# Kernel optimization log

Hardware: AMD Instinct MI355X
Metric: run time of the kernel (lower is better)

Reference implementation:

```python
import jax, jax.numpy as jnp
import numpy as np

N_NODES = 100000
N_EDGES = 3200000
NFEAT = 512
DIMS = [NFEAT, 12, 10, 8, 6, 4, 16]  # layer widths; 16 = nout


def setup_inputs() -> dict:
    key = jax.random.key(0)
    ks = jax.random.split(key, 16)
    inp = {
        "x": jax.random.normal(ks[0], (N_NODES, NFEAT), dtype=jnp.float32),
        "edge_index": jax.random.randint(ks[1], (2, N_EDGES), 0, N_NODES, dtype=jnp.int32),
        "edge_weight": jax.random.uniform(ks[2], (N_EDGES,), dtype=jnp.float32) * (1.0 / 32.0),
    }
    # GCN layer params: support = x @ W; out = adj @ support + b
    for i in range(6):
        fan_in, fan_out = DIMS[i], DIMS[i + 1]
        scale = 1.0 / np.sqrt(fan_in)
        inp[f"W{i+1}"] = jax.random.uniform(ks[3 + 2 * i], (fan_in, fan_out), dtype=jnp.float32, minval=-scale, maxval=scale)
        inp[f"b{i+1}"] = jax.random.uniform(ks[4 + 2 * i], (fan_out,), dtype=jnp.float32, minval=-scale, maxval=scale)
    return inp


def _gcn_layer(h, src, dst, w, W, b):
    # support = h @ W  -> [N, out]; out = A @ support + b via edge scatter-add
    support = h @ W
    msgs = w[:, None] * support[src]            # [E, out]
    agg = jax.ops.segment_sum(msgs, dst, num_segments=N_NODES)
    return agg + b


def reference(x, edge_index, edge_weight, W1, b1, W2, b2, W3, b3, W4, b4, W5, b5, W6, b6):
    src, dst = edge_index[0], edge_index[1]
    # Eval-mode forward: F.dropout(training=False) is identity.
    h = x
    for W, b in ((W1, b1), (W2, b2), (W3, b3), (W4, b4), (W5, b5), (W6, b6)):
        h = _gcn_layer(h, src, dst, edge_weight, W, b)
    return h
```

## Files before the change

### kernel.cpp

```cpp
#include <hip/hip_runtime.h>
#include <hip/hip_fp16.h>

constexpr int NF = 512;
constexpr int SCAN_B = 1024;
constexpr int DPB = 256;
constexpr int CHUNK = 16384;
constexpr int BMAX = 9216;
constexpr float WSCALE = 1048544.0f;
constexpr float WINV = 1.0f / 1048544.0f;

__device__ __forceinline__ float dot16(const float* a, const float* w, float acc) {
#pragma unroll
  for (int j = 0; j < 16; ++j) acc = fmaf(a[j], w[j], acc);
  return acc;
}

template <int COUT>
__global__ __launch_bounds__(256) void gemm_big_count_kernel(
    const float* __restrict__ x, const float* __restrict__ W,
    __half* __restrict__ sup, int n, const int* __restrict__ ei,
    int* __restrict__ cnt, int E, int nbuck, int nch) {
  __shared__ __align__(16) float smem[COUT * NF];
  if ((int)blockIdx.x < nch) {
    int* hist = (int*)smem;
    const int c = blockIdx.x;
    for (int b = threadIdx.x; b < nbuck; b += 256) hist[b] = 0;
    __syncthreads();
    const int base = c * CHUNK;
    for (int i = threadIdx.x; i < CHUNK; i += 256) {
      const int e = base + i;
      if (e < E) atomicAdd(&hist[ei[E + e] >> 8], 1);
    }
    __syncthreads();
    for (int b = threadIdx.x; b < nbuck; b += 256) cnt[b * nch + c] = hist[b];
    return;
  }

  float(*sW)[NF] = (float(*)[NF])smem;
  for (int i = threadIdx.x; i < COUT * NF; i += 256) {
    int c = i / NF, k = i - c * NF;
    sW[c][k] = W[(size_t)k * COUT + c];
  }
  __syncthreads();

  const int v = (blockIdx.x - nch) * 256 + threadIdx.x;
  if (v >= n) return;

  float acc[COUT];
#pragma unroll
  for (int c = 0; c < COUT; ++c) acc[c] = 0.f;

  const float4* xr = (const float4*)(x + (size_t)v * NF);
  float4 cur[4], nxt[4];
#pragma unroll
  for (int j = 0; j < 4; ++j) cur[j] = xr[j];
  for (int kb = 0; kb < NF / 16; ++kb) {
    const int kn = (kb + 1 < NF / 16) ? kb + 1 : kb;
#pragma unroll
    for (int j = 0; j < 4; ++j) nxt[j] = xr[kn * 4 + j];
    const float* af = (const float*)cur;
#pragma unroll
    for (int c = 0; c < COUT; ++c) {
      const float4* wr = (const float4*)(&sW[c][kb * 16]);
      float4 wq[4];
#pragma unroll
      for (int j = 0; j < 4; ++j) wq[j] = wr[j];
      acc[c] = dot16(af, (const float*)wq, acc[c]);
    }
#pragma unroll
    for (int j = 0; j < 4; ++j) cur[j] = nxt[j];
  }

  union { uint4 u; __half2 h[4]; } o1;
  union { uint2 u; __half2 h[2]; } o2;
#pragma unroll
  for (int g = 0; g < 4; ++g) o1.h[g] = __floats2half2_rn(acc[2 * g], acc[2 * g + 1]);
#pragma unroll
  for (int g = 0; g < 2; ++g) o2.h[g] = __floats2half2_rn(acc[8 + 2 * g], acc[9 + 2 * g]);
  __half* o = sup + (size_t)v * 16;
  *(uint4*)o = o1.u;
  *(uint2*)(o + 8) = o2.u;
}


__global__ __launch_bounds__(256) void scan1_kernel(const int* __restrict__ src,
                                                    int* __restrict__ dst,
                                                    int* __restrict__ bsums, int m) {
  __shared__ int s[256];
  const int t = threadIdx.x;
  const int idx = blockIdx.x * SCAN_B + t * 4;
  int4 d = {0, 0, 0, 0};
  if (idx + 3 < m) {
    d = *(const int4*)(src + idx);
  } else {
    if (idx + 0 < m) d.x = src[idx + 0];
    if (idx + 1 < m) d.y = src[idx + 1];
    if (idx + 2 < m) d.z = src[idx + 2];
    if (idx + 3 < m) d.w = src[idx + 3];
  }
  const int sum = d.x + d.y + d.z + d.w;
  s[t] = sum;
  __syncthreads();
  for (int off = 1; off < 256; off <<= 1) {
    int val = (t >= off) ? s[t - off] : 0;
    __syncthreads();
    s[t] += val;
    __syncthreads();
  }
  const int excl = s[t] - sum;
  if (t == 255) bsums[blockIdx.x] = s[255];
  if (idx + 0 < m) dst[idx + 0] = excl;
  if (idx + 1 < m) dst[idx + 1] = excl + d.x;
  if (idx + 2 < m) dst[idx + 2] = excl + d.x + d.y;
  if (idx + 3 < m) dst[idx + 3] = excl + d.x + d.y + d.z;
}

__global__ __launch_bounds__(256) void scan2_kernel(const int* __restrict__ bsums,
                                                    int* __restrict__ bscan, int nb) {
  __shared__ int s[256];
  const int t = threadIdx.x;
  const int v = (t < nb) ? bsums[t] : 0;
  s[t] = v;
  __syncthreads();
  for (int off = 1; off < 256; off <<= 1) {
    int val = (t >= off) ? s[t - off] : 0;
    __syncthreads();
    s[t] += val;
    __syncthreads();
  }
  if (t < nb) bscan[t] = s[t] - v;
}

__global__ __launch_bounds__(256) void scatterC_kernel(
    const int* __restrict__ ei, const float* __restrict__ ew,
    const int* __restrict__ offsp, const int* __restrict__ bscan,
    int2* __restrict__ pairs, int E, int nbuck, int nch) {
  __shared__ int cur[512];
  const int c = blockIdx.x;
  for (int b = threadIdx.x; b < nbuck; b += 256) {
    const int idx = b * nch + c;
    cur[b] = offsp[idx] + bscan[idx >> 10];
  }
  __syncthreads();
  const int base = c * CHUNK;
  for (int i = threadIdx.x; i < CHUNK; i += 256) {
    const int e = base + i;
    if (e >= E) break;
    const int s = ei[e];
    const int d = ei[E + e];
    const float w = ew[e];
    const int pos = atomicAdd(&cur[d >> 8], 1);
    pairs[pos] = make_int2(s | ((d & (DPB - 1)) << 17), __float_as_int(w));
  }
}

__global__ __launch_bounds__(256) void bucketD_kernel(
    const int* __restrict__ offsp, const int* __restrict__ bscan,
    const int2* __restrict__ pairs, unsigned* __restrict__ cpairs,
    int* __restrict__ rowptr, int n, int E, int nbuck, int nch) {
  __shared__ unsigned stage[BMAX];
  __shared__ int h[DPB];
  __shared__ int s[DPB];
  __shared__ int cur[DPB];
  const int b = blockIdx.x;
  const int t = threadIdx.x;
  if (b == 0 && t == 0) rowptr[n] = E;
  const int i0 = b * nch;
  const int base = offsp[i0] + bscan[i0 >> 10];
  int end;
  if (b + 1 < nbuck) {
    const int i1 = (b + 1) * nch;
    end = offsp[i1] + bscan[i1 >> 10];
  } else {
    end = E;
  }
  const int cnt = end - base;

  for (int i = t; i < DPB; i += 256) h[i] = 0;
  __syncthreads();
  for (int i = t; i < cnt; i += 256) {
    const int2 p = pairs[base + i];
    atomicAdd(&h[(p.x >> 17) & (DPB - 1)], 1);
  }
  __syncthreads();
  const int own = h[t];
  s[t] = own;
  __syncthreads();
  for (int off = 1; off < 256; off <<= 1) {
    int val = (t >= off) ? s[t - off] : 0;
    __syncthreads();
    s[t] += val;
    __syncthreads();
  }
  const int excl = s[t] - own;
  cur[t] = excl;
  const int dst = b * DPB + t;
  if (dst < n) rowptr[dst] = base + excl;
  __syncthreads();
  for (int i = t; i < cnt; i += 256) {
    const int2 p = pairs[base + i];
    const int r = atomicAdd(&cur[(p.x >> 17) & (DPB - 1)], 1);
    const float w = __int_as_float(p.y);
    const unsigned wq = (unsigned)__float2int_rn(w * WSCALE);
    if (r < BMAX) stage[r] = (unsigned)(p.x & 0x1FFFF) | (wq << 17);
  }
  __syncthreads();
  const int lim = cnt < BMAX ? cnt : BMAX;
  for (int i = t; i < lim; i += 256) cpairs[base + i] = stage[i];
}


template <int PIN, int CIN>
__device__ __forceinline__ void load_row_h(const __half* __restrict__ sup,
                                           unsigned p, float* hv, float* wout) {
  *wout = (float)(p >> 17) * WINV;
  const __half* hr = sup + (size_t)(p & 0x1FFFF) * PIN;
  __half2 h[6];
  if constexpr (PIN == 16) {
    union { uint4 u; __half2 h[4]; } a;
    union { uint2 u; __half2 h[2]; } b;
    a.u = *(const uint4*)hr;
    b.u = *(const uint2*)(hr + 8);
    h[0] = a.h[0]; h[1] = a.h[1]; h[2] = a.h[2]; h[3] = a.h[3];
    h[4] = b.h[0]; h[5] = b.h[1];
  } else if constexpr (PIN == 8) {
    union { uint4 u; __half2 h[4]; } a;
    a.u = *(const uint4*)hr;
    h[0] = a.h[0]; h[1] = a.h[1]; h[2] = a.h[2]; h[3] = a.h[3];
  } else {
    union { uint2 u; __half2 h[2]; } a;
    a.u = *(const uint2*)hr;
    h[0] = a.h[0]; h[1] = a.h[1];
  }
#pragma unroll
  for (int g = 0; g < CIN / 2; ++g) {
    float2 f = __half22float2(h[g]);
    hv[2 * g] = f.x;
    hv[2 * g + 1] = f.y;
  }
}

template <int PIN, int CIN, int COUT, int POUT, bool AGG_BIAS, bool OUT_BIAS,
          bool IDENT, typename TOUT>
__global__ __launch_bounds__(256) void pull_one_kernel(
    const int* __restrict__ rowptr, const unsigned* __restrict__ cp,
    const __half* __restrict__ sup, const float* __restrict__ bagg,
    const float* __restrict__ W, const float* __restrict__ bout,
    TOUT* __restrict__ outp, int n) {
  __shared__ float sW[IDENT ? 1 : CIN * 16];
  __shared__ float sba[16];
  __shared__ float sbo[16];
  const int tt = threadIdx.x;
  if constexpr (!IDENT) {
    for (int i = tt; i < CIN * 16; i += 256) {
      const int k = i >> 4, j = i & 15;
      sW[i] = (j < COUT) ? W[k * COUT + j] : 0.f;
    }
  }
  if constexpr (AGG_BIAS)
    if (tt < CIN) sba[tt] = bagg[tt];
  if constexpr (OUT_BIAS)
    if (tt < COUT) sbo[tt] = bout[tt];
  __syncthreads();

  const int gt = blockIdx.x * 256 + tt;
  const int v = gt >> 3;
  const int lane = gt & 7;
  if (v >= n) return;
  const int beg = rowptr[v];
  const int end = rowptr[v + 1];

  float acc[CIN];
#pragma unroll
  for (int c = 0; c < CIN; ++c) acc[c] = 0.f;

  for (int base = beg; base < end; base += 32) {
    const int i = base + 4 * lane;
    unsigned pq[4] = {0u, 0u, 0u, 0u};
    if (i < end) __builtin_memcpy(pq, cp + i, 16);
    const unsigned p0 = (i + 0 < end) ? pq[0] : 0u;
    const unsigned p1 = (i + 1 < end) ? pq[1] : 0u;
    const unsigned p2 = (i + 2 < end) ? pq[2] : 0u;
    const unsigned p3 = (i + 3 < end) ? pq[3] : 0u;
    float w0, w1, w2, w3, h0[CIN], h1[CIN], h2[CIN], h3[CIN];
    load_row_h<PIN, CIN>(sup, p0, h0, &w0);
    load_row_h<PIN, CIN>(sup, p1, h1, &w1);
    load_row_h<PIN, CIN>(sup, p2, h2, &w2);
    load_row_h<PIN, CIN>(sup, p3, h3, &w3);
#pragma unroll
    for (int c = 0; c < CIN; ++c) acc[c] = fmaf(w0, h0[c], acc[c]);
#pragma unroll
    for (int c = 0; c < CIN; ++c) acc[c] = fmaf(w1, h1[c], acc[c]);
#pragma unroll
    for (int c = 0; c < CIN; ++c) acc[c] = fmaf(w2, h2[c], acc[c]);
#pragma unroll
    for (int c = 0; c < CIN; ++c) acc[c] = fmaf(w3, h3[c], acc[c]);
  }

#pragma unroll
  for (int c = 0; c < CIN; ++c) {
    acc[c] += __shfl_xor(acc[c], 1);
    acc[c] += __shfl_xor(acc[c], 2);
    acc[c] += __shfl_xor(acc[c], 4);
    if constexpr (AGG_BIAS) acc[c] += sba[c];
  }

  if constexpr (IDENT) {
    if (lane == 0) {
      union { uint2 u; __half2 h[2]; } o;
      o.h[0] = __floats2half2_rn(acc[0], acc[1]);
      o.h[1] = __floats2half2_rn(acc[2], acc[3]);
      *(uint2*)((__half*)outp + (size_t)v * POUT) = o.u;
    }
  } else {
    if (lane * 4 < POUT) {
      const int col = lane * 4;
      float r[4];
#pragma unroll
      for (int j = 0; j < 4; ++j) {
        float a = OUT_BIAS ? sbo[col + j] : 0.f;
#pragma unroll
        for (int k = 0; k < CIN; ++k) a = fmaf(acc[k], sW[k * 16 + col + j], a);
        r[j] = a;
      }
      if constexpr (sizeof(TOUT) == 2) {
        union { uint2 u; __half2 h[2]; } o;
        o.h[0] = __floats2half2_rn(r[0], r[1]);
        o.h[1] = __floats2half2_rn(r[2], r[3]);
        *(uint2*)((__half*)outp + (size_t)v * POUT + col) = o.u;
      } else {
        float4 o;
        o.x = r[0]; o.y = r[1]; o.z = r[2]; o.w = r[3];
        *(float4*)((float*)outp + (size_t)v * POUT + col) = o;
      }
    }
  }
}

extern "C" void kernel_launch(void* const* d_in, const int* in_sizes, int n_in,
                              void* d_out, int out_size, void* d_ws,
                              size_t ws_size, hipStream_t stream) {
  const float* x = (const float*)d_in[0];
  const int* ei = (const int*)d_in[1];
  const float* ew = (const float*)d_in[2];
  const float* W1 = (const float*)d_in[3];
  const float* b1 = (const float*)d_in[4];
  const float* W2 = (const float*)d_in[5];
  const float* b2 = (const float*)d_in[6];
  const float* W3 = (const float*)d_in[7];
  const float* b3 = (const float*)d_in[8];
  const float* W4 = (const float*)d_in[9];
  const float* b4 = (const float*)d_in[10];
  const float* W5 = (const float*)d_in[11];
  const float* b5 = (const float*)d_in[12];
  const float* W6 = (const float*)d_in[13];
  const float* b6 = (const float*)d_in[14];
  float* out = (float*)d_out;

  const int n = in_sizes[0] / NF;
  const int E = in_sizes[2];

  const int nbuck = (n + DPB - 1) / DPB;
  const int nch = (E + CHUNK - 1) / CHUNK;
  const int M = nbuck * nch;
  const int Mpad = (M + 3) & ~3;

  __half* A = (__half*)d_ws;
  __half* B = A + (size_t)n * 16;
  int* cnt = (int*)(B + (size_t)n * 16);
  int* offs = cnt + Mpad;
  int* bsums = offs + Mpad;
  int* bscan = bsums + 256;
  int* rowptr = bscan + 256;
  uintptr_t up = (uintptr_t)(rowptr + n + 1);
  up = (up + 15) & ~(uintptr_t)15;
  unsigned* cpairs = (unsigned*)up;
  int2* pairs = (int2*)(cpairs + E);

  const int gn256 = (n + 255) / 256;
  const int nsb = (M + SCAN_B - 1) / SCAN_B;
  const int gq8 = (n * 8 + 255) / 256;

  gemm_big_count_kernel<12>
      <<<nch + gn256, 256, 0, stream>>>(x, W1, A, n, ei, cnt, E, nbuck, nch);
  scan1_kernel<<<nsb, 256, 0, stream>>>(cnt, offs, bsums, M);
  scan2_kernel<<<1, 256, 0, stream>>>(bsums, bscan, nsb);
  scatterC_kernel<<<nch, 256, 0, stream>>>(ei, ew, offs, bscan, pairs, E, nbuck, nch);
  bucketD_kernel<<<nbuck, 256, 0, stream>>>(offs, bscan, pairs, cpairs, rowptr,
                                            n, E, nbuck, nch);

  pull_one_kernel<16, 12, 10, 16, true, false, false, __half>
      <<<gq8, 256, 0, stream>>>(rowptr, cpairs, A, b1, W2, nullptr, B, n);
  pull_one_kernel<16, 10, 8, 8, true, false, false, __half>
      <<<gq8, 256, 0, stream>>>(rowptr, cpairs, B, b2, W3, nullptr, A, n);
  pull_one_kernel<8, 8, 6, 8, true, false, false, __half>
      <<<gq8, 256, 0, stream>>>(rowptr, cpairs, A, b3, W4, nullptr, B, n);
  pull_one_kernel<8, 6, 4, 4, true, false, false, __half>
      <<<gq8, 256, 0, stream>>>(rowptr, cpairs, B, b4, W5, nullptr, A, n);
  pull_one_kernel<4, 4, 4, 4, true, false, true, __half>
      <<<gq8, 256, 0, stream>>>(rowptr, cpairs, A, b5, nullptr, nullptr, B, n);
  pull_one_kernel<4, 4, 16, 16, false, true, false, float>
      <<<gq8, 256, 0, stream>>>(rowptr, cpairs, B, nullptr, W6, b6, out, n);
}
```

Before: 272.7 us.

## Split 16-wide gather rows across thread pairs and stride edge loads per lane

Adds a pull kernel for the two 16-column layers in which 16 lanes serve one node, and each lane pair splits a row into two 8-half 16-byte loads. The results are then exchanged with shuffles before the small output matmul. The generic pull kernel also switches from each lane taking 4 consecutive edges to a lane-strided pattern with two edges in flight per iteration. This aims to shorten per-lane serial gather chains and improve load vectorisation, at the cost of more threads, more shuffles and less memory-level parallelism per lane.

```diff
diff --git a/kernel.cpp b/kernel.cpp
--- a/kernel.cpp
+++ b/kernel.cpp
@@ -210,20 +210,108 @@
 }
 
 
+template <int CIN, int COUT, int POUT>
+__global__ __launch_bounds__(256) void pull_paired_kernel(
+    const int* __restrict__ rowptr, const unsigned* __restrict__ cp,
+    const __half* __restrict__ sup, const float* __restrict__ bagg,
+    const float* __restrict__ W, __half* __restrict__ outp, int n) {
+  __shared__ float sW[CIN * 16];
+  __shared__ float sba[16];
+  const int tt = threadIdx.x;
+  for (int i = tt; i < CIN * 16; i += 256) {
+    const int k = i >> 4, j = i & 15;
+    sW[i] = (j < COUT) ? W[k * COUT + j] : 0.f;
+  }
+  if (tt < CIN) sba[tt] = bagg[tt];
+  __syncthreads();
+
+  const int gt = blockIdx.x * 256 + tt;
+  const int v = gt >> 4;
+  const int lane = gt & 15;
+  const int slot = lane >> 1;
+  const int par = lane & 1;
+  if (v >= n) return;
+  const int beg = rowptr[v];
+  const int end = rowptr[v + 1];
+
+  float acc[8];
+#pragma unroll
+  for (int c = 0; c < 8; ++c) acc[c] = 0.f;
+
+  auto gather = [&](unsigned p, float* h8, float* wout) {
+    *wout = (float)(p >> 17) * WINV;
+    const __half* hr = sup + (size_t)(p & 0x1FFFF) * 16 + par * 8;
+    union { uint4 u; __half2 h[4]; } a;
+    a.u = *(const uint4*)hr;
+#pragma unroll
+    for (int g = 0; g < 4; ++g) {
+      float2 f = __half22float2(a.h[g]);
+      h8[2 * g] = f.x;
+      h8[2 * g + 1] = f.y;
+    }
+  };
+
+  int i = beg + slot;
+  for (; i + 8 < end; i += 16) {
+    const unsigned p0 = cp[i];
+    const unsigned p1 = cp[i + 8];
+    float w0, w1, h0[8], h1[8];
+    gather(p0, h0, &w0);
+    gather(p1, h1, &w1);
+#pragma unroll
+    for (int c = 0; c < 8; ++c) acc[c] = fmaf(w0, h0[c], acc[c]);
+#pragma unroll
+    for (int c = 0; c < 8; ++c) acc[c] = fmaf(w1, h1[c], acc[c]);
+  }
+  if (i < end) {
+    const unsigned p0 = cp[i];
+    float w0, h0[8];
+    gather(p0, h0, &w0);
+#pragma unroll
+    for (int c = 0; c < 8; ++c) acc[c] = fmaf(w0, h0[c], acc[c]);
+  }
+
+#pragma unroll
+  for (int c = 0; c < 8; ++c) {
+    acc[c] += __shfl_xor(acc[c], 2);
+    acc[c] += __shfl_xor(acc[c], 4);
+    acc[c] += __shfl_xor(acc[c], 8);
+  }
+  float h[16];
+#pragma unroll
+  for (int c = 0; c < 8; ++c) {
+    const float o = __shfl_xor(acc[c], 1);
+    h[c] = par ? o : acc[c];
+    h[8 + c] = par ? acc[c] : o;
+  }
+#pragma unroll
+  for (int c = 0; c < CIN; ++c) h[c] += sba[c];
+
+  if (lane * 4 < POUT) {
+    const int col = lane * 4;
+    float r[4];
+#pragma unroll
+    for (int j = 0; j < 4; ++j) {
+      float a = 0.f;
+#pragma unroll
+      for (int k = 0; k < CIN; ++k) a = fmaf(h[k], sW[k * 16 + col + j], a);
+      r[j] = a;
+    }
+    union { uint2 u; __half2 h2[2]; } o;
+    o.h2[0] = __floats2half2_rn(r[0], r[1]);
+    o.h2[1] = __floats2half2_rn(r[2], r[3]);
+    *(uint2*)(outp + (size_t)v * POUT + col) = o.u;
+  }
+}
+
+
 template <int PIN, int CIN>
 __device__ __forceinline__ void load_row_h(const __half* __restrict__ sup,
                                            unsigned p, float* hv, float* wout) {
   *wout = (float)(p >> 17) * WINV;
   const __half* hr = sup + (size_t)(p & 0x1FFFF) * PIN;
-  __half2 h[6];
-  if constexpr (PIN == 16) {
-    union { uint4 u; __half2 h[4]; } a;
-    union { uint2 u; __half2 h[2]; } b;
-    a.u = *(const uint4*)hr;
-    b.u = *(const uint2*)(hr + 8);
-    h[0] = a.h[0]; h[1] = a.h[1]; h[2] = a.h[2]; h[3] = a.h[3];
-    h[4] = b.h[0]; h[5] = b.h[1];
-  } else if constexpr (PIN == 8) {
+  __half2 h[4];
+  if constexpr (PIN == 8) {
     union { uint4 u; __half2 h[4]; } a;
     a.u = *(const uint4*)hr;
     h[0] = a.h[0]; h[1] = a.h[1]; h[2] = a.h[2]; h[3] = a.h[3];
@@ -274,27 +362,24 @@
 #pragma unroll
   for (int c = 0; c < CIN; ++c) acc[c] = 0.f;
 
-  for (int base = beg; base < end; base += 32) {
-    const int i = base + 4 * lane;
-    unsigned pq[4] = {0u, 0u, 0u, 0u};
-    if (i < end) __builtin_memcpy(pq, cp + i, 16);
-    const unsigned p0 = (i + 0 < end) ? pq[0] : 0u;
-    const unsigned p1 = (i + 1 < end) ? pq[1] : 0u;
-    const unsigned p2 = (i + 2 < end) ? pq[2] : 0u;
-    const unsigned p3 = (i + 3 < end) ? pq[3] : 0u;
-    float w0, w1, w2, w3, h0[CIN], h1[CIN], h2[CIN], h3[CIN];
+  int i = beg + lane;
+  for (; i + 8 < end; i += 16) {
+    const unsigned p0 = cp[i];
+    const unsigned p1 = cp[i + 8];
+    float w0, w1, h0[CIN], h1[CIN];
     load_row_h<PIN, CIN>(sup, p0, h0, &w0);
     load_row_h<PIN, CIN>(sup, p1, h1, &w1);
-    load_row_h<PIN, CIN>(sup, p2, h2, &w2);
-    load_row_h<PIN, CIN>(sup, p3, h3, &w3);
 #pragma unroll
     for (int c = 0; c < CIN; ++c) acc[c] = fmaf(w0, h0[c], acc[c]);
 #pragma unroll
     for (int c = 0; c < CIN; ++c) acc[c] = fmaf(w1, h1[c], acc[c]);
-#pragma unroll
-    for (int c = 0; c < CIN; ++c) acc[c] = fmaf(w2, h2[c], acc[c]);
-#pragma unroll
-    for (int c = 0; c < CIN; ++c) acc[c] = fmaf(w3, h3[c], acc[c]);
+  }
+  if (i < end) {
+    const unsigned p0 = cp[i];
+    float w0, h0[CIN];
+    load_row_h<PIN, CIN>(sup, p0, h0, &w0);
+#pragma unroll
+    for (int c = 0; c < CIN; ++c) acc[c] = fmaf(w0, h0[c], acc[c]);
   }
 
 #pragma unroll
@@ -380,6 +465,7 @@
   const int gn256 = (n + 255) / 256;
   const int nsb = (M + SCAN_B - 1) / SCAN_B;
   const int gq8 = (n * 8 + 255) / 256;
+  const int gq16 = (n * 16 + 255) / 256;
 
   gemm_big_count_kernel<12>
       <<<nch + gn256, 256, 0, stream>>>(x, W1, A, n, ei, cnt, E, nbuck, nch);
@@ -389,10 +475,10 @@
   bucketD_kernel<<<nbuck, 256, 0, stream>>>(offs, bscan, pairs, cpairs, rowptr,
                                             n, E, nbuck, nch);
 
-  pull_one_kernel<16, 12, 10, 16, true, false, false, __half>
-      <<<gq8, 256, 0, stream>>>(rowptr, cpairs, A, b1, W2, nullptr, B, n);
-  pull_one_kernel<16, 10, 8, 8, true, false, false, __half>
-      <<<gq8, 256, 0, stream>>>(rowptr, cpairs, B, b2, W3, nullptr, A, n);
+  pull_paired_kernel<12, 10, 16>
+      <<<gq16, 256, 0, stream>>>(rowptr, cpairs, A, b1, W2, B, n);
+  pull_paired_kernel<10, 8, 8>
+      <<<gq16, 256, 0, stream>>>(rowptr, cpairs, B, b2, W3, A, n);
   pull_one_kernel<8, 8, 6, 8, true, false, false, __half>
       <<<gq8, 256, 0, stream>>>(rowptr, cpairs, A, b3, W4, nullptr, B, n);
   pull_one_kernel<8, 6, 4, 4, true, false, false, __half>
```

Measured after the change: 266.7 us. 1.02x faster.

## Split GEMM K-dimension across four waves and interleave pull-kernel edge loads

Applied to the files above, without the earlier changes.

The first-layer GEMM now handles 64 nodes per block, with each of four waves covering a quarter of the 512-wide K dimension. Partial sums are reduced through shared memory, which quadruples the block count for more parallelism and latency hiding, at the cost of an extra LDS reduction and a sync. The pull aggregation kernel also replaces its 4-wide contiguous edge-pair loads with strided per-lane loads of 2 edges per iteration plus a tail. This lowers register pressure and gives coalesced loads across lanes, but issues fewer loads in flight per thread.

```diff
diff --git a/kernel.cpp b/kernel.cpp
--- a/kernel.cpp
+++ b/kernel.cpp
@@ -20,9 +20,10 @@
     const float* __restrict__ x, const float* __restrict__ W,
     __half* __restrict__ sup, int n, const int* __restrict__ ei,
     int* __restrict__ cnt, int E, int nbuck, int nch) {
-  __shared__ __align__(16) float smem[COUT * NF];
+  __shared__ __align__(16) float sW[COUT * NF];
+  __shared__ __align__(16) float part[4][COUT][64];
   if ((int)blockIdx.x < nch) {
-    int* hist = (int*)smem;
+    int* hist = (int*)sW;
     const int c = blockIdx.x;
     for (int b = threadIdx.x; b < nbuck; b += 256) hist[b] = 0;
     __syncthreads();
@@ -36,32 +37,35 @@
     return;
   }
 
-  float(*sW)[NF] = (float(*)[NF])smem;
   for (int i = threadIdx.x; i < COUT * NF; i += 256) {
     int c = i / NF, k = i - c * NF;
-    sW[c][k] = W[(size_t)k * COUT + c];
-  }
-  __syncthreads();
-
-  const int v = (blockIdx.x - nch) * 256 + threadIdx.x;
-  if (v >= n) return;
+    sW[c * NF + k] = W[(size_t)k * COUT + c];
+  }
+  __syncthreads();
+
+  const int w = threadIdx.x >> 6;
+  const int lane = threadIdx.x & 63;
+  const int vbase = (blockIdx.x - nch) * 64;
+  const int v = vbase + lane;
+  const int ve = (v < n) ? v : (n - 1);
 
   float acc[COUT];
 #pragma unroll
   for (int c = 0; c < COUT; ++c) acc[c] = 0.f;
 
-  const float4* xr = (const float4*)(x + (size_t)v * NF);
+  const float4* xr = (const float4*)(x + (size_t)ve * NF) + w * 32;
   float4 cur[4], nxt[4];
 #pragma unroll
   for (int j = 0; j < 4; ++j) cur[j] = xr[j];
-  for (int kb = 0; kb < NF / 16; ++kb) {
-    const int kn = (kb + 1 < NF / 16) ? kb + 1 : kb;
+  for (int kb = 0; kb < 8; ++kb) {
+    const int kn = (kb + 1 < 8) ? kb + 1 : kb;
 #pragma unroll
     for (int j = 0; j < 4; ++j) nxt[j] = xr[kn * 4 + j];
     const float* af = (const float*)cur;
+    const int kq = w * 8 + kb;
 #pragma unroll
     for (int c = 0; c < COUT; ++c) {
-      const float4* wr = (const float4*)(&sW[c][kb * 16]);
+      const float4* wr = (const float4*)(&sW[c * NF + kq * 16]);
       float4 wq[4];
 #pragma unroll
       for (int j = 0; j < 4; ++j) wq[j] = wr[j];
@@ -71,15 +75,26 @@
     for (int j = 0; j < 4; ++j) cur[j] = nxt[j];
   }
 
-  union { uint4 u; __half2 h[4]; } o1;
-  union { uint2 u; __half2 h[2]; } o2;
-#pragma unroll
-  for (int g = 0; g < 4; ++g) o1.h[g] = __floats2half2_rn(acc[2 * g], acc[2 * g + 1]);
-#pragma unroll
-  for (int g = 0; g < 2; ++g) o2.h[g] = __floats2half2_rn(acc[8 + 2 * g], acc[9 + 2 * g]);
-  __half* o = sup + (size_t)v * 16;
-  *(uint4*)o = o1.u;
-  *(uint2*)(o + 8) = o2.u;
+#pragma unroll
+  for (int c = 0; c < COUT; ++c) part[w][c][lane] = acc[c];
+  __syncthreads();
+
+  if (w == 0 && v < n) {
+    float r[COUT];
+#pragma unroll
+    for (int c = 0; c < COUT; ++c)
+      r[c] = part[0][c][lane] + part[1][c][lane] + part[2][c][lane] +
+             part[3][c][lane];
+    union { uint4 u; __half2 h[4]; } o1;
+    union { uint2 u; __half2 h[2]; } o2;
+#pragma unroll
+    for (int g = 0; g < 4; ++g) o1.h[g] = __floats2half2_rn(r[2 * g], r[2 * g + 1]);
+#pragma unroll
+    for (int g = 0; g < 2; ++g) o2.h[g] = __floats2half2_rn(r[8 + 2 * g], r[9 + 2 * g]);
+    __half* o = sup + (size_t)v * 16;
+    *(uint4*)o = o1.u;
+    *(uint2*)(o + 8) = o2.u;
+  }
 }
 
 
@@ -274,27 +289,24 @@
 #pragma unroll
   for (int c = 0; c < CIN; ++c) acc[c] = 0.f;
 
-  for (int base = beg; base < end; base += 32) {
-    const int i = base + 4 * lane;
-    unsigned pq[4] = {0u, 0u, 0u, 0u};
-    if (i < end) __builtin_memcpy(pq, cp + i, 16);
-    const unsigned p0 = (i + 0 < end) ? pq[0] : 0u;
-    const unsigned p1 = (i + 1 < end) ? pq[1] : 0u;
-    const unsigned p2 = (i + 2 < end) ? pq[2] : 0u;
-    const unsigned p3 = (i + 3 < end) ? pq[3] : 0u;
-    float w0, w1, w2, w3, h0[CIN], h1[CIN], h2[CIN], h3[CIN];
+  int i = beg + lane;
+  for (; i + 8 < end; i += 16) {
+    const unsigned p0 = cp[i];
+    const unsigned p1 = cp[i + 8];
+    float w0, w1, h0[CIN], h1[CIN];
     load_row_h<PIN, CIN>(sup, p0, h0, &w0);
     load_row_h<PIN, CIN>(sup, p1, h1, &w1);
-    load_row_h<PIN, CIN>(sup, p2, h2, &w2);
-    load_row_h<PIN, CIN>(sup, p3, h3, &w3);
 #pragma unroll
     for (int c = 0; c < CIN; ++c) acc[c] = fmaf(w0, h0[c], acc[c]);
 #pragma unroll
     for (int c = 0; c < CIN; ++c) acc[c] = fmaf(w1, h1[c], acc[c]);
-#pragma unroll
-    for (int c = 0; c < CIN; ++c) acc[c] = fmaf(w2, h2[c], acc[c]);
-#pragma unroll
-    for (int c = 0; c < CIN; ++c) acc[c] = fmaf(w3, h3[c], acc[c]);
+  }
+  if (i < end) {
+    const unsigned p0 = cp[i];
+    float w0, h0[CIN];
+    load_row_h<PIN, CIN>(sup, p0, h0, &w0);
+#pragma unroll
+    for (int c = 0; c < CIN; ++c) acc[c] = fmaf(w0, h0[c], acc[c]);
   }
 
 #pragma unroll
@@ -377,12 +389,12 @@
   unsigned* cpairs = (unsigned*)up;
   int2* pairs = (int2*)(cpairs + E);
 
-  const int gn256 = (n + 255) / 256;
+  const int gnb = (n + 63) / 64;
   const int nsb = (M + SCAN_B - 1) / SCAN_B;
   const int gq8 = (n * 8 + 255) / 256;
 
   gemm_big_count_kernel<12>
-      <<<nch + gn256, 256, 0, stream>>>(x, W1, A, n, ei, cnt, E, nbuck, nch);
+      <<<nch + gnb, 256, 0, stream>>>(x, W1, A, n, ei, cnt, E, nbuck, nch);
   scan1_kernel<<<nsb, 256, 0, stream>>>(cnt, offs, bsums, M);
   scan2_kernel<<<1, 256, 0, stream>>>(bsums, bscan, nsb);
   scatterC_kernel<<<nch, 256, 0, stream>>>(ei, ew, offs, bscan, pairs, E, nbuck, nch);
```

Result: faster. 261.9 us (-4.0%).
